# Kernel optimization log

Hardware: AMD Instinct MI355X
Metric: run time of the kernel (lower is better)

## Reference

```python
import jax, jax.numpy as jnp
import numpy as np

H = 2048          # hidden_size
I_MOE = 1408      # moe_intermediate_size (per expert)
I_SH = 5632       # shared_expert_intermediate_size
E = 8             # num_experts
TOP_K = 2         # num_experts_per_tok
B, S = 1, 2048


def setup_inputs() -> dict:
    key = jax.random.key(0)
    ks = jax.random.split(key, 7)
    sc = 0.02
    return {
        "hidden_states": jax.random.normal(ks[0], (B, S, H), jnp.float32),
        "W_router": jax.random.normal(ks[1], (E, H), jnp.float32) * sc,      # gate.weight
        "W_sgate": jax.random.normal(ks[2], (1, H), jnp.float32) * sc,       # shared_expert_gate.weight
        "Ws_gate_up": jax.random.normal(ks[3], (H, 2 * I_SH), jnp.float32) * sc,  # shared expert merged gate/up
        "Ws_down": jax.random.normal(ks[4], (I_SH, H), jnp.float32) * sc,
        "We_gate_up": jax.random.normal(ks[5], (E, H, 2 * I_MOE), jnp.float32) * sc,  # stacked expert gate/up
        "We_down": jax.random.normal(ks[6], (E, I_MOE, H), jnp.float32) * sc,
    }


def _silu_and_mul(gu, inter):
    # gate_up layout: [..., 2*inter] -> silu(gate) * up, matching SiluAndMul
    return jax.nn.silu(gu[..., :inter]) * gu[..., inter:]


def reference(hidden_states, W_router, W_sgate, Ws_gate_up, Ws_down, We_gate_up, We_down):
    orig_shape = hidden_states.shape
    x = hidden_states.reshape(-1, H)                     # [T, H]
    T = x.shape[0]

    # --- router: softmax in fp32 then top-k (NOT renormalized, as in source) ---
    logits = x @ W_router.T                              # [T, E]
    probs = jax.nn.softmax(logits.astype(jnp.float32), axis=-1)
    rw, sel = jax.lax.top_k(probs, TOP_K)                # [T, K]
    rw = rw.astype(x.dtype)

    # sparse combine matrix [T, E]: routing weight where selected, else 0
    combine = jnp.zeros((T, E), x.dtype).at[jnp.arange(T)[:, None], sel].add(rw)

    # --- shared expert ---
    sh = _silu_and_mul(x @ Ws_gate_up, I_SH) @ Ws_down    # [T, H]
    shared_out = sh * jax.nn.sigmoid(x @ W_sgate.T)       # [T, H]

    # --- experts: dense dispatch (math-identical to gather/MLP/index_add loop) ---
    gu = jnp.einsum('th,ehi->eti', x, We_gate_up)         # [E, T, 2*I_MOE]
    h = _silu_and_mul(gu, I_MOE)                          # [E, T, I_MOE]
    eo = jnp.einsum('eti,eih->eth', h, We_down)           # [E, T, H]
    sparse_out = jnp.einsum('eth,te->th', eo, combine)    # [T, H]

    return (shared_out + sparse_out).reshape(orig_shape)
```

## Files before the change

### kernel.cpp

```cpp
#include <hip/hip_runtime.h>
#include <cstdio>


#define H_DIM 2048
#define IMOE  1408
#define ISH   5632
#define NEXP  8
#define T_TOK 2048
#define TK_TOT (T_TOK * 2)

typedef __attribute__((ext_vector_type(8))) short short8;
typedef __attribute__((ext_vector_type(8))) __bf16 bf16x8;
typedef __attribute__((ext_vector_type(4))) float f32x4;

__device__ __forceinline__ float bf2f(unsigned short u) {
  union { unsigned int i; float f; } v; v.i = ((unsigned int)u) << 16; return v.f;
}
__device__ __forceinline__ unsigned short f2bf(float f) {
  union { float f; unsigned int i; } v; v.f = f;
  unsigned int x = v.i;
  return (unsigned short)((x + 0x7fffu + ((x >> 16) & 1u)) >> 16);
}

__device__ __forceinline__ f32x4 MFMA16(short8 a, short8 b, f32x4 c) {
  return __builtin_amdgcn_mfma_f32_16x16x32_bf16(
      __builtin_bit_cast(bf16x8, a), __builtin_bit_cast(bf16x8, b), c, 0, 0, 0);
}

__device__ __forceinline__ void gload_lds16(const unsigned short* g, unsigned short* l) {
  __builtin_amdgcn_global_load_lds(
      (const __attribute__((address_space(1))) unsigned int*)g,
      (__attribute__((address_space(3))) unsigned int*)l, 16, 0, 0);
}

__device__ __forceinline__ float silu_f(float x) { return x / (1.0f + __expf(-x)); }

#define SBAR()   asm volatile("s_barrier" ::: "memory")
#define VMCNT(n) asm volatile("s_waitcnt vmcnt(" #n ")" ::: "memory")


template <bool ILV>
__global__ __launch_bounds__(256)
void transpose_cvt_kernel(const float* __restrict__ src, unsigned short* __restrict__ dst,
                          int R, int C, int I, long sStride, long dStride) {
  src += (long)blockIdx.z * sStride;
  dst += (long)blockIdx.z * dStride;
  __shared__ float tile[32][33];
  int tx = threadIdx.x, ty = threadIdx.y;
  int x = blockIdx.x * 32 + tx;
  int yb = blockIdx.y * 32;
#pragma unroll
  for (int j = 0; j < 4; j++) {
    int y = yb + ty + j * 8;
    tile[ty + j * 8][tx] = src[(long)y * C + x];
  }
  __syncthreads();
  int r = yb + tx;
#pragma unroll
  for (int j = 0; j < 4; j++) {
    int c = blockIdx.x * 32 + ty + j * 8;
    int cd = ILV ? (c < I ? 2 * c : 2 * (c - I) + 1) : c;
    dst[(long)cd * R + r] = f2bf(tile[tx][ty + j * 8]);
  }
}

__global__ __launch_bounds__(256)
void cvt_x_kernel(const float* __restrict__ x, unsigned short* __restrict__ xb, int total4) {
  int i = blockIdx.x * 256 + threadIdx.x;
  if (i >= total4) return;
  float4 v = ((const float4*)x)[i];
  ushort4 o;
  o.x = f2bf(v.x); o.y = f2bf(v.y); o.z = f2bf(v.z); o.w = f2bf(v.w);
  ((ushort4*)xb)[i] = o;
}


__global__ __launch_bounds__(256)
void router_kernel(const float* __restrict__ x, const float* __restrict__ Wr,
                   const float* __restrict__ Wsg, float* __restrict__ rw,
                   int* __restrict__ sel, float* __restrict__ sgate_sig,
                   int* __restrict__ counts) {
  int t = blockIdx.x;
  const float* xr = x + (long)t * H_DIM;
  float p[9];
#pragma unroll
  for (int e = 0; e < 9; e++) p[e] = 0.0f;
  for (int h = threadIdx.x; h < H_DIM; h += 256) {
    float xv = xr[h];
#pragma unroll
    for (int e = 0; e < 8; e++) p[e] += xv * Wr[e * H_DIM + h];
    p[8] += xv * Wsg[h];
  }
#pragma unroll
  for (int e = 0; e < 9; e++)
    for (int off = 32; off > 0; off >>= 1)
      p[e] += __shfl_down(p[e], off, 64);
  __shared__ float red[4][9];
  int wave = threadIdx.x >> 6, lane = threadIdx.x & 63;
  if (lane == 0) {
#pragma unroll
    for (int e = 0; e < 9; e++) red[wave][e] = p[e];
  }
  __syncthreads();
  if (threadIdx.x == 0) {
    float lg[9];
#pragma unroll
    for (int e = 0; e < 9; e++) lg[e] = red[0][e] + red[1][e] + red[2][e] + red[3][e];
    float m = lg[0];
#pragma unroll
    for (int e = 1; e < 8; e++) m = fmaxf(m, lg[e]);
    float pr[8], s = 0.0f;
#pragma unroll
    for (int e = 0; e < 8; e++) { pr[e] = expf(lg[e] - m); s += pr[e]; }
    float inv = 1.0f / s;
#pragma unroll
    for (int e = 0; e < 8; e++) pr[e] *= inv;
    int i0 = 0;
#pragma unroll
    for (int e = 1; e < 8; e++) if (pr[e] > pr[i0]) i0 = e;
    int i1 = (i0 == 0) ? 1 : 0;
#pragma unroll
    for (int e = 0; e < 8; e++) if (e != i0 && pr[e] > pr[i1]) i1 = e;
    rw[t * 2] = pr[i0]; rw[t * 2 + 1] = pr[i1];
    sel[t * 2] = i0;    sel[t * 2 + 1] = i1;
    sgate_sig[t] = 1.0f / (1.0f + expf(-lg[8]));
    atomicAdd(&counts[i0], 1);
    atomicAdd(&counts[i1], 1);
  }
}

__global__ void scan_kernel(const int* __restrict__ counts, int* __restrict__ offsets) {
  if (threadIdx.x == 0 && blockIdx.x == 0) {
    int s = 0;
    for (int e = 0; e < NEXP; e++) { offsets[e] = s; s += counts[e]; }
    offsets[NEXP] = s;
  }
}

__global__ __launch_bounds__(256)
void scatter_kernel(const int* __restrict__ sel, const int* __restrict__ offsets,
                    int* __restrict__ cursor, int* __restrict__ tok_of_slot,
                    int* __restrict__ slot_of_tok) {
  int t = blockIdx.x * 256 + threadIdx.x;
  if (t >= T_TOK) return;
#pragma unroll
  for (int k = 0; k < 2; k++) {
    int e = sel[t * 2 + k];
    int pos = atomicAdd(&cursor[e], 1);
    int slot = offsets[e] + pos;
    tok_of_slot[slot] = t;
    slot_of_tok[t * 2 + k] = slot;
  }
}

__global__ __launch_bounds__(256)
void gather_kernel(const unsigned short* __restrict__ xbf, const int* __restrict__ tok,
                   unsigned short* __restrict__ xg) {
  int i = blockIdx.x * 256 + threadIdx.x;
  int slot = i >> 8, c8 = i & 255;
  long src = (long)tok[slot] * H_DIM + c8 * 8;
  ulonglong2 v = *(const ulonglong2*)(xbf + src);
  ((ulonglong2*)xg)[i] = v;
}

template <int EPI, bool EXPERT>
__global__ __launch_bounds__(512, 2)
void gemm2p_kernel(const unsigned short* __restrict__ A,
                   const unsigned short* __restrict__ BT,
                   void* __restrict__ Cv,
                   int N, int Kld, int KLEN, int M,
                   const int* __restrict__ counts, const int* __restrict__ offsets,
                   const float* __restrict__ rowscale, long bt_estride) {
  __shared__ unsigned short lds8[65536];

  int cnt = M, rowbase = 0, k0 = 0;
  const unsigned short* bt = BT;
  if constexpr (EXPERT) {
    int e = blockIdx.z;
    cnt = counts[e];
    rowbase = offsets[e];
    bt += (long)e * bt_estride;
  } else {
    k0 = blockIdx.z * KLEN;
  }
  int row0 = blockIdx.x * 256;
  if (row0 >= cnt) return;
  int col0 = blockIdx.y * 256;

  int tid = threadIdx.x, wave = tid >> 6, lane = tid & 63;
  int NT = KLEN / 64;

  const unsigned short* aSrc[4];
  const unsigned short* bSrc[4];
#pragma unroll
  for (int s = 0; s < 4; s++) {
    int r = s * 64 + (tid >> 3);
    int g = (tid & 7) ^ (r & 7);
    long ar = row0 + r;
    if (ar > cnt - 1) ar = cnt - 1;
    ar += rowbase;
    aSrc[s] = A + ar * (long)Kld + k0 + g * 8;
    bSrc[s] = bt + (long)(col0 + r) * Kld + k0 + g * 8;
  }

  int wr = wave >> 2, wc = wave & 3;
  int fr = lane & 15, fg = lane >> 4;
  int aOff[8][2], bOff[4][2];
#pragma unroll
  for (int ks = 0; ks < 2; ks++) {
    int q = ((ks * 4 + fg) ^ (fr & 7)) * 8;
#pragma unroll
    for (int m = 0; m < 8; m++) aOff[m][ks] = (wr * 128 + m * 16 + fr) * 64 + q;
#pragma unroll
    for (int n = 0; n < 4; n++) bOff[n][ks] = (wc * 64 + n * 16 + fr) * 64 + q;
  }

#define STAGE(p, t) do { long kk = (long)(t) * 64; \
    _Pragma("unroll") for (int s = 0; s < 4; s++) { \
      gload_lds16(aSrc[s] + kk, &lds8[(p) * 16384 + s * 4096 + wave * 512]); \
      gload_lds16(bSrc[s] + kk, &lds8[32768 + (p) * 16384 + s * 4096 + wave * 512]); \
    } } while (0)

  f32x4 acc[8][4] = {};

  STAGE(0, 0);
  VMCNT(0);
  SBAR();

  for (int t = 0; t < NT; t++) {
    int p = t & 1;
    if (t + 1 < NT) STAGE(p ^ 1, t + 1);
#pragma unroll
    for (int ks = 0; ks < 2; ks++) {
      short8 aF[8], bF[4];
#pragma unroll
      for (int m = 0; m < 8; m++) aF[m] = *(const short8*)&lds8[p * 16384 + aOff[m][ks]];
#pragma unroll
      for (int n = 0; n < 4; n++) bF[n] = *(const short8*)&lds8[32768 + p * 16384 + bOff[n][ks]];
      __builtin_amdgcn_s_setprio(1);
#pragma unroll
      for (int m = 0; m < 8; m++)
#pragma unroll
        for (int n = 0; n < 4; n++)
          acc[m][n] = MFMA16(aF[m], bF[n], acc[m][n]);
      __builtin_amdgcn_s_setprio(0);
    }
    VMCNT(0);
    SBAR();
  }

  int rowguard = cnt - row0;
#pragma unroll
  for (int m = 0; m < 8; m++) {
    int rl = wr * 128 + m * 16 + fg * 4;
#pragma unroll
    for (int n = 0; n < 4; n++) {
      int cg = col0 + wc * 64 + n * 16 + fr;
      f32x4 v = acc[m][n];
#pragma unroll
      for (int j = 0; j < 4; j++) {
        int r = rl + j;
        float pv = __shfl_xor(v[j], 1);
        if (r < rowguard) {
          long orow = (long)rowbase + row0 + r;
          if constexpr (EPI == 1) {
            unsafeAtomicAdd(&((float*)Cv)[orow * (long)N + cg], v[j] * rowscale[orow]);
          } else if constexpr (EPI == 2) {
            ((float*)Cv)[orow * (long)N + cg] = v[j];
          } else {
            if (!(fr & 1)) {
              float hval = silu_f(v[j]) * pv;
              ((unsigned short*)Cv)[orow * (long)(N >> 1) + (cg >> 1)] = f2bf(hval);
            }
          }
        }
      }
    }
  }
#undef STAGE
}


__global__ __launch_bounds__(256)
void combine_kernel(float* __restrict__ out, const float* __restrict__ eo,
                    const int* __restrict__ slot_of_tok, const float* __restrict__ rw) {
  int i = blockIdx.x * 256 + threadIdx.x;
  const int h4n = H_DIM / 4;
  if (i >= T_TOK * h4n) return;
  int t = i / h4n;
  int h4 = i - t * h4n;
  int s0 = slot_of_tok[t * 2], s1 = slot_of_tok[t * 2 + 1];
  float w0 = rw[t * 2], w1 = rw[t * 2 + 1];
  float4 o = ((float4*)out)[i];
  float4 a = ((const float4*)eo)[(long)s0 * h4n + h4];
  float4 b = ((const float4*)eo)[(long)s1 * h4n + h4];
  o.x += w0 * a.x + w1 * b.x;
  o.y += w0 * a.y + w1 * b.y;
  o.z += w0 * a.z + w1 * b.z;
  o.w += w0 * a.w + w1 * b.w;
  ((float4*)out)[i] = o;
}


extern "C" void kernel_launch(void* const* d_in, const int* in_sizes, int n_in,
                              void* d_out, int out_size, void* d_ws, size_t ws_size,
                              hipStream_t stream) {
  (void)in_sizes; (void)n_in; (void)out_size;
  const float* x    = (const float*)d_in[0];
  const float* Wr   = (const float*)d_in[1];
  const float* Wsg  = (const float*)d_in[2];
  const float* Wsgu = (const float*)d_in[3];
  const float* Wsd  = (const float*)d_in[4];
  const float* Wegu = (const float*)d_in[5];
  const float* Wed  = (const float*)d_in[6];
  float* out = (float*)d_out;

  char* ws = (char*)d_ws;
  size_t off = 0;
  auto alloc = [&](size_t b) { size_t o = off; off += (b + 255) & ~(size_t)255; return o; };

  size_t o_xbf   = alloc((size_t)T_TOK * H_DIM * 2);
  size_t o_WsguT = alloc((size_t)2 * ISH * H_DIM * 2);
  size_t o_WsdT  = alloc((size_t)H_DIM * ISH * 2);
  size_t o_WeguT = alloc((size_t)NEXP * 2 * IMOE * H_DIM * 2);
  size_t o_WedT  = alloc((size_t)NEXP * H_DIM * IMOE * 2);
  size_t o_hsh   = alloc((size_t)T_TOK * ISH * 2);
  size_t o_he    = alloc((size_t)TK_TOT * IMOE * 2);
  size_t o_xg    = alloc((size_t)TK_TOT * H_DIM * 2);
  size_t o_ints  = alloc(256);
  size_t o_rw    = alloc((size_t)TK_TOT * 4);
  size_t o_sel   = alloc((size_t)TK_TOT * 4);
  size_t o_sg    = alloc((size_t)T_TOK * 4);
  size_t o_tok   = alloc((size_t)TK_TOT * 4);
  size_t o_s2t   = alloc((size_t)TK_TOT * 4);

  if (off > ws_size) {
    fprintf(stderr, "[moe kernel] workspace too small: need %zu have %zu\n", off, ws_size);
    return;
  }

  unsigned short* xbf   = (unsigned short*)(ws + o_xbf);
  unsigned short* WsguT = (unsigned short*)(ws + o_WsguT);
  unsigned short* WsdT  = (unsigned short*)(ws + o_WsdT);
  unsigned short* WeguT = (unsigned short*)(ws + o_WeguT);
  unsigned short* WedT  = (unsigned short*)(ws + o_WedT);
  unsigned short* h_sh  = (unsigned short*)(ws + o_hsh);
  unsigned short* h_e   = (unsigned short*)(ws + o_he);
  unsigned short* xg    = (unsigned short*)(ws + o_xg);
  float* eo             = (float*)(ws + o_WsguT);

  int* ints    = (int*)(ws + o_ints);
  int* counts  = ints;
  int* cursor  = ints + 8;
  int* offsets = ints + 16;
  float* rw    = (float*)(ws + o_rw);
  int* sel     = (int*)(ws + o_sel);
  float* sgate = (float*)(ws + o_sg);
  int* tok     = (int*)(ws + o_tok);
  int* s2t     = (int*)(ws + o_s2t);

  dim3 tb(32, 8, 1);

  hipMemsetAsync(ints, 0, 64, stream);
  hipMemsetAsync(out, 0, (size_t)T_TOK * H_DIM * 4, stream);

  cvt_x_kernel<<<(T_TOK * H_DIM / 4) / 256, 256, 0, stream>>>(x, xbf, T_TOK * H_DIM / 4);
  router_kernel<<<T_TOK, 256, 0, stream>>>(x, Wr, Wsg, rw, sel, sgate, counts);
  scan_kernel<<<1, 64, 0, stream>>>(counts, offsets);
  scatter_kernel<<<(T_TOK + 255) / 256, 256, 0, stream>>>(sel, offsets, cursor, tok, s2t);
  gather_kernel<<<TK_TOT, 256, 0, stream>>>(xbf, tok, xg);


  transpose_cvt_kernel<true><<<dim3(2 * ISH / 32, H_DIM / 32, 1), tb, 0, stream>>>(
      Wsgu, WsguT, H_DIM, 2 * ISH, ISH, 0, 0);
  gemm2p_kernel<3, false><<<dim3(T_TOK / 256, 2 * ISH / 256, 1), 512, 0, stream>>>(
      xbf, WsguT, h_sh, 2 * ISH, H_DIM, H_DIM, T_TOK, nullptr, nullptr, nullptr, 0);

  transpose_cvt_kernel<true><<<dim3(2 * IMOE / 32, H_DIM / 32, NEXP), tb, 0, stream>>>(
      Wegu, WeguT, H_DIM, 2 * IMOE, IMOE, (long)H_DIM * 2 * IMOE, (long)2 * IMOE * H_DIM);
  gemm2p_kernel<3, true><<<dim3(T_TOK / 256, 2 * IMOE / 256, NEXP), 512, 0, stream>>>(
      xg, WeguT, h_e, 2 * IMOE, H_DIM, H_DIM, 0, counts, offsets, nullptr,
      (long)2 * IMOE * H_DIM);

  transpose_cvt_kernel<false><<<dim3(H_DIM / 32, ISH / 32, 1), tb, 0, stream>>>(
      Wsd, WsdT, ISH, H_DIM, 0, 0, 0);
  gemm2p_kernel<1, false><<<dim3(T_TOK / 256, H_DIM / 256, 4), 512, 0, stream>>>(
      h_sh, WsdT, out, H_DIM, ISH, ISH / 4, T_TOK, nullptr, nullptr, sgate, 0);

  transpose_cvt_kernel<false><<<dim3(H_DIM / 32, IMOE / 32, NEXP), tb, 0, stream>>>(
      Wed, WedT, IMOE, H_DIM, 0, (long)IMOE * H_DIM, (long)H_DIM * IMOE);
  gemm2p_kernel<2, true><<<dim3(T_TOK / 256, H_DIM / 256, NEXP), 512, 0, stream>>>(
      h_e, WedT, eo, H_DIM, IMOE, IMOE, 0, counts, offsets, nullptr,
      (long)H_DIM * IMOE);

  combine_kernel<<<(T_TOK * H_DIM / 4) / 256, 256, 0, stream>>>(out, eo, s2t, rw);
}
```

Before: 775.9 us.

## Merge GEMMs and weight conversions into horizontally fused mega-kernels

Replaces the serial sequence of transpose/convert and GEMM launches with three mega-kernels. Each one runs a GEMM phase's tiles alongside the weight conversion needed by a later phase, or runs the shared and expert down-projections together, so memory-bound conversion overlaps compute-bound matmul. The x-to-bf16 conversion is folded into the router kernel, and GEMM tile order is swizzled by XCD. In exchange, conversion blocks are now large 512-thread blocks using the full 128KB LDS allocation, which may limit occupancy and balance.

```diff
diff --git a/kernel.cpp b/kernel.cpp
--- a/kernel.cpp
+++ b/kernel.cpp
@@ -38,154 +38,25 @@
 #define SBAR()   asm volatile("s_barrier" ::: "memory")
 #define VMCNT(n) asm volatile("s_waitcnt vmcnt(" #n ")" ::: "memory")
 
-
-template <bool ILV>
-__global__ __launch_bounds__(256)
-void transpose_cvt_kernel(const float* __restrict__ src, unsigned short* __restrict__ dst,
-                          int R, int C, int I, long sStride, long dStride) {
-  src += (long)blockIdx.z * sStride;
-  dst += (long)blockIdx.z * dStride;
-  __shared__ float tile[32][33];
-  int tx = threadIdx.x, ty = threadIdx.y;
-  int x = blockIdx.x * 32 + tx;
-  int yb = blockIdx.y * 32;
-#pragma unroll
-  for (int j = 0; j < 4; j++) {
-    int y = yb + ty + j * 8;
-    tile[ty + j * 8][tx] = src[(long)y * C + x];
-  }
-  __syncthreads();
-  int r = yb + tx;
-#pragma unroll
-  for (int j = 0; j < 4; j++) {
-    int c = blockIdx.x * 32 + ty + j * 8;
-    int cd = ILV ? (c < I ? 2 * c : 2 * (c - I) + 1) : c;
-    dst[(long)cd * R + r] = f2bf(tile[tx][ty + j * 8]);
-  }
-}
-
-__global__ __launch_bounds__(256)
-void cvt_x_kernel(const float* __restrict__ x, unsigned short* __restrict__ xb, int total4) {
-  int i = blockIdx.x * 256 + threadIdx.x;
-  if (i >= total4) return;
-  float4 v = ((const float4*)x)[i];
-  ushort4 o;
-  o.x = f2bf(v.x); o.y = f2bf(v.y); o.z = f2bf(v.z); o.w = f2bf(v.w);
-  ((ushort4*)xb)[i] = o;
-}
-
-
-__global__ __launch_bounds__(256)
-void router_kernel(const float* __restrict__ x, const float* __restrict__ Wr,
-                   const float* __restrict__ Wsg, float* __restrict__ rw,
-                   int* __restrict__ sel, float* __restrict__ sgate_sig,
-                   int* __restrict__ counts) {
-  int t = blockIdx.x;
-  const float* xr = x + (long)t * H_DIM;
-  float p[9];
-#pragma unroll
-  for (int e = 0; e < 9; e++) p[e] = 0.0f;
-  for (int h = threadIdx.x; h < H_DIM; h += 256) {
-    float xv = xr[h];
-#pragma unroll
-    for (int e = 0; e < 8; e++) p[e] += xv * Wr[e * H_DIM + h];
-    p[8] += xv * Wsg[h];
-  }
-#pragma unroll
-  for (int e = 0; e < 9; e++)
-    for (int off = 32; off > 0; off >>= 1)
-      p[e] += __shfl_down(p[e], off, 64);
-  __shared__ float red[4][9];
-  int wave = threadIdx.x >> 6, lane = threadIdx.x & 63;
-  if (lane == 0) {
-#pragma unroll
-    for (int e = 0; e < 9; e++) red[wave][e] = p[e];
-  }
-  __syncthreads();
-  if (threadIdx.x == 0) {
-    float lg[9];
-#pragma unroll
-    for (int e = 0; e < 9; e++) lg[e] = red[0][e] + red[1][e] + red[2][e] + red[3][e];
-    float m = lg[0];
-#pragma unroll
-    for (int e = 1; e < 8; e++) m = fmaxf(m, lg[e]);
-    float pr[8], s = 0.0f;
-#pragma unroll
-    for (int e = 0; e < 8; e++) { pr[e] = expf(lg[e] - m); s += pr[e]; }
-    float inv = 1.0f / s;
-#pragma unroll
-    for (int e = 0; e < 8; e++) pr[e] *= inv;
-    int i0 = 0;
-#pragma unroll
-    for (int e = 1; e < 8; e++) if (pr[e] > pr[i0]) i0 = e;
-    int i1 = (i0 == 0) ? 1 : 0;
-#pragma unroll
-    for (int e = 0; e < 8; e++) if (e != i0 && pr[e] > pr[i1]) i1 = e;
-    rw[t * 2] = pr[i0]; rw[t * 2 + 1] = pr[i1];
-    sel[t * 2] = i0;    sel[t * 2 + 1] = i1;
-    sgate_sig[t] = 1.0f / (1.0f + expf(-lg[8]));
-    atomicAdd(&counts[i0], 1);
-    atomicAdd(&counts[i1], 1);
-  }
-}
-
-__global__ void scan_kernel(const int* __restrict__ counts, int* __restrict__ offsets) {
-  if (threadIdx.x == 0 && blockIdx.x == 0) {
-    int s = 0;
-    for (int e = 0; e < NEXP; e++) { offsets[e] = s; s += counts[e]; }
-    offsets[NEXP] = s;
-  }
-}
-
-__global__ __launch_bounds__(256)
-void scatter_kernel(const int* __restrict__ sel, const int* __restrict__ offsets,
-                    int* __restrict__ cursor, int* __restrict__ tok_of_slot,
-                    int* __restrict__ slot_of_tok) {
-  int t = blockIdx.x * 256 + threadIdx.x;
-  if (t >= T_TOK) return;
-#pragma unroll
-  for (int k = 0; k < 2; k++) {
-    int e = sel[t * 2 + k];
-    int pos = atomicAdd(&cursor[e], 1);
-    int slot = offsets[e] + pos;
-    tok_of_slot[slot] = t;
-    slot_of_tok[t * 2 + k] = slot;
-  }
-}
-
-__global__ __launch_bounds__(256)
-void gather_kernel(const unsigned short* __restrict__ xbf, const int* __restrict__ tok,
-                   unsigned short* __restrict__ xg) {
-  int i = blockIdx.x * 256 + threadIdx.x;
-  int slot = i >> 8, c8 = i & 255;
-  long src = (long)tok[slot] * H_DIM + c8 * 8;
-  ulonglong2 v = *(const ulonglong2*)(xbf + src);
-  ((ulonglong2*)xg)[i] = v;
-}
-
 template <int EPI, bool EXPERT>
-__global__ __launch_bounds__(512, 2)
-void gemm2p_kernel(const unsigned short* __restrict__ A,
-                   const unsigned short* __restrict__ BT,
-                   void* __restrict__ Cv,
-                   int N, int Kld, int KLEN, int M,
-                   const int* __restrict__ counts, const int* __restrict__ offsets,
-                   const float* __restrict__ rowscale, long bt_estride) {
-  __shared__ unsigned short lds8[65536];
-
+__device__ __forceinline__ void gemm_core(
+    const unsigned short* __restrict__ A, const unsigned short* __restrict__ BT,
+    void* __restrict__ Cv, int N, int Kld, int KLEN, int M,
+    const int* __restrict__ counts, const int* __restrict__ offsets,
+    const float* __restrict__ rowscale, long bt_estride,
+    int bx, int by, int bz, unsigned short* lds8) {
   int cnt = M, rowbase = 0, k0 = 0;
   const unsigned short* bt = BT;
   if constexpr (EXPERT) {
-    int e = blockIdx.z;
-    cnt = counts[e];
-    rowbase = offsets[e];
-    bt += (long)e * bt_estride;
+    cnt = counts[bz];
+    rowbase = offsets[bz];
+    bt += (long)bz * bt_estride;
   } else {
-    k0 = blockIdx.z * KLEN;
-  }
-  int row0 = blockIdx.x * 256;
+    k0 = bz * KLEN;
+  }
+  int row0 = bx * 256;
   if (row0 >= cnt) return;
-  int col0 = blockIdx.y * 256;
+  int col0 = by * 256;
 
   int tid = threadIdx.x, wave = tid >> 6, lane = tid & 63;
   int NT = KLEN / 64;
@@ -280,6 +151,216 @@
 #undef STAGE
 }
 
+__device__ __forceinline__ void cvt_job(
+    const float* __restrict__ src, unsigned short* __restrict__ dst, int j,
+    int Ytiles, int Ctiles, int Cc, int Rr, int I, long sStride, long dStride,
+    void* ldsraw) {
+  float (*tile)[33] = (float(*)[33])ldsraw;
+  int tid = threadIdx.x;
+  int tx = tid & 31, ty = tid >> 5;
+  int perz = Ytiles * Ctiles;
+  for (int it = 0; it < 64; ++it) {
+    int tl = j * 64 + it;
+    int tz = tl / perz, rem = tl - tz * perz;
+    int tyc = rem / Ctiles, txc = rem - tyc * Ctiles;
+    const float* s = src + (long)tz * sStride;
+    unsigned short* d = dst + (long)tz * dStride;
+    int yb = tyc * 32, x0 = txc * 32;
+    __syncthreads();
+#pragma unroll
+    for (int jj = 0; jj < 2; jj++) {
+      int y = ty + jj * 16;
+      tile[y][tx] = s[(long)(yb + y) * Cc + x0 + tx];
+    }
+    __syncthreads();
+#pragma unroll
+    for (int jj = 0; jj < 2; jj++) {
+      int c = x0 + ty + jj * 16;
+      int cd = I ? (c < I ? 2 * c : 2 * (c - I) + 1) : c;
+      d[(long)cd * Rr + yb + tx] = f2bf(tile[tx][ty + jj * 16]);
+    }
+  }
+}
+
+template <bool ILV>
+__global__ __launch_bounds__(256)
+void transpose_cvt_kernel(const float* __restrict__ src, unsigned short* __restrict__ dst,
+                          int R, int C, int I) {
+  __shared__ float tile[32][33];
+  int tx = threadIdx.x, ty = threadIdx.y;
+  int x = blockIdx.x * 32 + tx;
+  int yb = blockIdx.y * 32;
+#pragma unroll
+  for (int j = 0; j < 4; j++) {
+    int y = yb + ty + j * 8;
+    tile[ty + j * 8][tx] = src[(long)y * C + x];
+  }
+  __syncthreads();
+  int r = yb + tx;
+#pragma unroll
+  for (int j = 0; j < 4; j++) {
+    int c = blockIdx.x * 32 + ty + j * 8;
+    int cd = ILV ? (c < I ? 2 * c : 2 * (c - I) + 1) : c;
+    dst[(long)cd * R + r] = f2bf(tile[tx][ty + j * 8]);
+  }
+}
+
+
+__global__ __launch_bounds__(256)
+void router_kernel(const float* __restrict__ x, const float* __restrict__ Wr,
+                   const float* __restrict__ Wsg, float* __restrict__ rw,
+                   int* __restrict__ sel, float* __restrict__ sgate_sig,
+                   int* __restrict__ counts, unsigned short* __restrict__ xbf) {
+  int t = blockIdx.x;
+  const float* xr = x + (long)t * H_DIM;
+  unsigned short* xo = xbf + (long)t * H_DIM;
+  float p[9];
+#pragma unroll
+  for (int e = 0; e < 9; e++) p[e] = 0.0f;
+  for (int h = threadIdx.x; h < H_DIM; h += 256) {
+    float xv = xr[h];
+    xo[h] = f2bf(xv);
+#pragma unroll
+    for (int e = 0; e < 8; e++) p[e] += xv * Wr[e * H_DIM + h];
+    p[8] += xv * Wsg[h];
+  }
+#pragma unroll
+  for (int e = 0; e < 9; e++)
+    for (int off = 32; off > 0; off >>= 1)
+      p[e] += __shfl_down(p[e], off, 64);
+  __shared__ float red[4][9];
+  int wave = threadIdx.x >> 6, lane = threadIdx.x & 63;
+  if (lane == 0) {
+#pragma unroll
+    for (int e = 0; e < 9; e++) red[wave][e] = p[e];
+  }
+  __syncthreads();
+  if (threadIdx.x == 0) {
+    float lg[9];
+#pragma unroll
+    for (int e = 0; e < 9; e++) lg[e] = red[0][e] + red[1][e] + red[2][e] + red[3][e];
+    float m = lg[0];
+#pragma unroll
+    for (int e = 1; e < 8; e++) m = fmaxf(m, lg[e]);
+    float pr[8], s = 0.0f;
+#pragma unroll
+    for (int e = 0; e < 8; e++) { pr[e] = expf(lg[e] - m); s += pr[e]; }
+    float inv = 1.0f / s;
+#pragma unroll
+    for (int e = 0; e < 8; e++) pr[e] *= inv;
+    int i0 = 0;
+#pragma unroll
+    for (int e = 1; e < 8; e++) if (pr[e] > pr[i0]) i0 = e;
+    int i1 = (i0 == 0) ? 1 : 0;
+#pragma unroll
+    for (int e = 0; e < 8; e++) if (e != i0 && pr[e] > pr[i1]) i1 = e;
+    rw[t * 2] = pr[i0]; rw[t * 2 + 1] = pr[i1];
+    sel[t * 2] = i0;    sel[t * 2 + 1] = i1;
+    sgate_sig[t] = 1.0f / (1.0f + expf(-lg[8]));
+    atomicAdd(&counts[i0], 1);
+    atomicAdd(&counts[i1], 1);
+  }
+}
+
+__global__ void scan_kernel(const int* __restrict__ counts, int* __restrict__ offsets) {
+  if (threadIdx.x == 0 && blockIdx.x == 0) {
+    int s = 0;
+    for (int e = 0; e < NEXP; e++) { offsets[e] = s; s += counts[e]; }
+    offsets[NEXP] = s;
+  }
+}
+
+__global__ __launch_bounds__(256)
+void scatter_kernel(const int* __restrict__ sel, const int* __restrict__ offsets,
+                    int* __restrict__ cursor, int* __restrict__ tok_of_slot,
+                    int* __restrict__ slot_of_tok) {
+  int t = blockIdx.x * 256 + threadIdx.x;
+  if (t >= T_TOK) return;
+#pragma unroll
+  for (int k = 0; k < 2; k++) {
+    int e = sel[t * 2 + k];
+    int pos = atomicAdd(&cursor[e], 1);
+    int slot = offsets[e] + pos;
+    tok_of_slot[slot] = t;
+    slot_of_tok[t * 2 + k] = slot;
+  }
+}
+
+__global__ __launch_bounds__(256)
+void gather_kernel(const unsigned short* __restrict__ xbf, const int* __restrict__ tok,
+                   unsigned short* __restrict__ xg) {
+  int i = blockIdx.x * 256 + threadIdx.x;
+  int slot = i >> 8, c8 = i & 255;
+  long src = (long)tok[slot] * H_DIM + c8 * 8;
+  ulonglong2 v = *(const ulonglong2*)(xbf + src);
+  ((ulonglong2*)xg)[i] = v;
+}
+
+
+__global__ __launch_bounds__(512, 2)
+void megaB_kernel(const unsigned short* __restrict__ xbf,
+                  const unsigned short* __restrict__ WsguT,
+                  unsigned short* __restrict__ h_sh,
+                  const float* __restrict__ Wegu, unsigned short* __restrict__ WeguT,
+                  const float* __restrict__ Wsd, unsigned short* __restrict__ WsdT) {
+  __shared__ unsigned short lds8[65536];
+  int b = blockIdx.x;
+  if (b < 352) {
+    int s = (b & 7) * 44 + (b >> 3);
+    gemm_core<3, false>(xbf, WsguT, h_sh, 2 * ISH, H_DIM, H_DIM, T_TOK,
+                        nullptr, nullptr, nullptr, 0, s % 8, s / 8, 0, lds8);
+  } else if (b < 1056) {
+    cvt_job(Wegu, WeguT, b - 352, 64, 88, 2 * IMOE, H_DIM, IMOE,
+            (long)H_DIM * 2 * IMOE, (long)2 * IMOE * H_DIM, lds8);
+  } else {
+    cvt_job(Wsd, WsdT, b - 1056, 176, 64, H_DIM, ISH, 0, 0, 0, lds8);
+  }
+}
+
+__global__ __launch_bounds__(512, 2)
+void megaC_kernel(const unsigned short* __restrict__ xg,
+                  const unsigned short* __restrict__ WeguT,
+                  unsigned short* __restrict__ h_e,
+                  const int* __restrict__ counts, const int* __restrict__ offsets,
+                  const float* __restrict__ Wed, unsigned short* __restrict__ WedT) {
+  __shared__ unsigned short lds8[65536];
+  int b = blockIdx.x;
+  if (b < 704) {
+    int s = (b & 7) * 88 + (b >> 3);
+    int e = s / 88, r2 = s % 88;
+    gemm_core<3, true>(xg, WeguT, h_e, 2 * IMOE, H_DIM, H_DIM, 0,
+                       counts, offsets, nullptr, (long)2 * IMOE * H_DIM,
+                       r2 % 8, r2 / 8, e, lds8);
+  } else {
+    cvt_job(Wed, WedT, b - 704, 44, 64, H_DIM, IMOE,
+            0, (long)IMOE * H_DIM, (long)H_DIM * IMOE, lds8);
+  }
+}
+
+__global__ __launch_bounds__(512, 2)
+void megaD_kernel(const unsigned short* __restrict__ h_sh,
+                  const unsigned short* __restrict__ WsdT,
+                  float* __restrict__ out, const float* __restrict__ sgate,
+                  const unsigned short* __restrict__ h_e,
+                  const unsigned short* __restrict__ WedT,
+                  float* __restrict__ eo,
+                  const int* __restrict__ counts, const int* __restrict__ offsets) {
+  __shared__ unsigned short lds8[65536];
+  int o = blockIdx.x;
+  int s = (o & 7) * 96 + (o >> 3);
+  if (s < 256) {
+    gemm_core<1, false>(h_sh, WsdT, out, H_DIM, ISH, ISH / 4, T_TOK,
+                        nullptr, nullptr, sgate, 0,
+                        s % 8, (s >> 3) & 7, s >> 6, lds8);
+  } else {
+    int s2 = s - 256;
+    int e = s2 >> 6, r2 = s2 & 63;
+    gemm_core<2, true>(h_e, WedT, eo, H_DIM, IMOE, IMOE, 0,
+                       counts, offsets, nullptr, (long)H_DIM * IMOE,
+                       r2 % 8, r2 / 8, e, lds8);
+  }
+}
+
 
 __global__ __launch_bounds__(256)
 void combine_kernel(float* __restrict__ out, const float* __restrict__ eo,
@@ -359,39 +440,23 @@
   int* tok     = (int*)(ws + o_tok);
   int* s2t     = (int*)(ws + o_s2t);
 
-  dim3 tb(32, 8, 1);
-
   hipMemsetAsync(ints, 0, 64, stream);
   hipMemsetAsync(out, 0, (size_t)T_TOK * H_DIM * 4, stream);
 
-  cvt_x_kernel<<<(T_TOK * H_DIM / 4) / 256, 256, 0, stream>>>(x, xbf, T_TOK * H_DIM / 4);
-  router_kernel<<<T_TOK, 256, 0, stream>>>(x, Wr, Wsg, rw, sel, sgate, counts);
+  transpose_cvt_kernel<true><<<dim3(2 * ISH / 32, H_DIM / 32, 1), dim3(32, 8, 1), 0, stream>>>(
+      Wsgu, WsguT, H_DIM, 2 * ISH, ISH);
+
+  router_kernel<<<T_TOK, 256, 0, stream>>>(x, Wr, Wsg, rw, sel, sgate, counts, xbf);
   scan_kernel<<<1, 64, 0, stream>>>(counts, offsets);
   scatter_kernel<<<(T_TOK + 255) / 256, 256, 0, stream>>>(sel, offsets, cursor, tok, s2t);
   gather_kernel<<<TK_TOT, 256, 0, stream>>>(xbf, tok, xg);
 
-
-  transpose_cvt_kernel<true><<<dim3(2 * ISH / 32, H_DIM / 32, 1), tb, 0, stream>>>(
-      Wsgu, WsguT, H_DIM, 2 * ISH, ISH, 0, 0);
-  gemm2p_kernel<3, false><<<dim3(T_TOK / 256, 2 * ISH / 256, 1), 512, 0, stream>>>(
-      xbf, WsguT, h_sh, 2 * ISH, H_DIM, H_DIM, T_TOK, nullptr, nullptr, nullptr, 0);
-
-  transpose_cvt_kernel<true><<<dim3(2 * IMOE / 32, H_DIM / 32, NEXP), tb, 0, stream>>>(
-      Wegu, WeguT, H_DIM, 2 * IMOE, IMOE, (long)H_DIM * 2 * IMOE, (long)2 * IMOE * H_DIM);
-  gemm2p_kernel<3, true><<<dim3(T_TOK / 256, 2 * IMOE / 256, NEXP), 512, 0, stream>>>(
-      xg, WeguT, h_e, 2 * IMOE, H_DIM, H_DIM, 0, counts, offsets, nullptr,
-      (long)2 * IMOE * H_DIM);
-
-  transpose_cvt_kernel<false><<<dim3(H_DIM / 32, ISH / 32, 1), tb, 0, stream>>>(
-      Wsd, WsdT, ISH, H_DIM, 0, 0, 0);
-  gemm2p_kernel<1, false><<<dim3(T_TOK / 256, H_DIM / 256, 4), 512, 0, stream>>>(
-      h_sh, WsdT, out, H_DIM, ISH, ISH / 4, T_TOK, nullptr, nullptr, sgate, 0);
-
-  transpose_cvt_kernel<false><<<dim3(H_DIM / 32, IMOE / 32, NEXP), tb, 0, stream>>>(
-      Wed, WedT, IMOE, H_DIM, 0, (long)IMOE * H_DIM, (long)H_DIM * IMOE);
-  gemm2p_kernel<2, true><<<dim3(T_TOK / 256, H_DIM / 256, NEXP), 512, 0, stream>>>(
-      h_e, WedT, eo, H_DIM, IMOE, IMOE, 0, counts, offsets, nullptr,
-      (long)H_DIM * IMOE);
+  megaB_kernel<<<1232, 512, 0, stream>>>(xbf, WsguT, h_sh, Wegu, WeguT, Wsd, WsdT);
+
+  megaC_kernel<<<1056, 512, 0, stream>>>(xg, WeguT, h_e, counts, offsets, Wed, WedT);
+
+  megaD_kernel<<<768, 512, 0, stream>>>(h_sh, WsdT, out, sgate, h_e, WedT, eo,
+                                        counts, offsets);
 
   combine_kernel<<<(T_TOK * H_DIM / 4) / 256, 256, 0, stream>>>(out, eo, s2t, rw);
 }
```

After: 889.9 us. +14.7%, slower.
